# Optimization experiments

Hardware: AMD Instinct MI355X
Metric: run time of the kernel (lower is better)

The kernel has to match this reference:

```python
import jax, jax.numpy as jnp
import numpy as np

B, T, C = 4, 2048, 1024
H = 16
HS = C // H

def setup_inputs() -> dict:
    key = jax.random.key(0)
    ks = jax.random.split(key, 5)
    s = 0.02
    return {
        "x": jax.random.normal(ks[0], (B, T, C), dtype=jnp.float32),
        "c_attn_w": jax.random.normal(ks[1], (C, 3 * C), dtype=jnp.float32) * s,
        "c_attn_b": jax.random.normal(ks[2], (3 * C,), dtype=jnp.float32) * s,
        "c_proj_w": jax.random.normal(ks[3], (C, C), dtype=jnp.float32) * s,
        "c_proj_b": jax.random.normal(ks[4], (C,), dtype=jnp.float32) * s,
    }

def reference(x, c_attn_w, c_attn_b, c_proj_w, c_proj_b):
    b, t, c = x.shape
    qkv = x @ c_attn_w + c_attn_b                       # (B,T,3C)
    q, k, v = jnp.split(qkv, 3, axis=2)
    # (B,T,C) -> (B,H,T,hs)
    q = q.reshape(b, t, H, HS).transpose(0, 2, 1, 3)
    k = k.reshape(b, t, H, HS).transpose(0, 2, 1, 3)
    v = v.reshape(b, t, H, HS).transpose(0, 2, 1, 3)
    scale = 1.0 / np.sqrt(HS).astype(np.float32)
    attn = jnp.einsum("bhqd,bhkd->bhqk", q, k) * scale  # (B,H,T,T)
    causal = jnp.tril(jnp.ones((t, t), dtype=bool))
    attn = jnp.where(causal[None, None, :, :], attn, -jnp.inf)
    attn = jax.nn.softmax(attn, axis=-1)
    y = jnp.einsum("bhqk,bhkd->bhqd", attn, v)          # (B,H,T,hs)
    y = y.transpose(0, 2, 1, 3).reshape(b, t, c)        # (B,T,C)
    return y @ c_proj_w + c_proj_b
```

## Files before the change

### kernel.cpp

```cpp
#include <hip/hip_runtime.h>

typedef __attribute__((ext_vector_type(8))) _Float16 h8;
typedef __attribute__((ext_vector_type(4))) _Float16 h4;
typedef __attribute__((ext_vector_type(4))) float f4;
typedef __attribute__((ext_vector_type(16))) float f16x;
typedef __attribute__((ext_vector_type(4))) unsigned u4;

#define MFMA16(a,b,c) __builtin_amdgcn_mfma_f32_16x16x32_f16(a,b,c,0,0,0)
#define MFMA32(a,b,c) __builtin_amdgcn_mfma_f32_32x32x16_f16(a,b,c,0,0,0)

__device__ inline void gload16(const void* g, void* l) {
    __builtin_amdgcn_global_load_lds(
        (const __attribute__((address_space(1))) void*)g,
        (__attribute__((address_space(3))) void*)l, 16, 0, 0);
}

__device__ inline float swap_half(float x) { return __shfl_xor(x, 32, 64); }

__global__ __launch_bounds__(256) void k_f32_to_f16(const float* __restrict__ in,
                                                    _Float16* __restrict__ out, int n4) {
    int i = blockIdx.x * 256 + threadIdx.x;
    if (i < n4) {
        float4 v = ((const float4*)in)[i];
        h4 h;
        h[0] = (_Float16)v.x; h[1] = (_Float16)v.y;
        h[2] = (_Float16)v.z; h[3] = (_Float16)v.w;
        ((h4*)out)[i] = h;
    }
}

__global__ __launch_bounds__(256) void k_transpose_f16(const float* __restrict__ W,
                                                       _Float16* __restrict__ Wt,
                                                       int K, int N) {
    __shared__ float tile[64 * 68];
    const int k0 = blockIdx.x * 64, n0 = blockIdx.y * 64;
    const int t = threadIdx.x;
    const int tr = t >> 4;
    const int tc = t & 15;
#pragma unroll
    for (int i = 0; i < 4; ++i) {
        int r = tr + i * 16;
        float4 v = *(const float4*)(W + (size_t)(k0 + r) * N + n0 + tc * 4);
        *(float4*)(&tile[r * 68 + tc * 4]) = v;
    }
    __syncthreads();
#pragma unroll
    for (int i = 0; i < 4; ++i) {
        int nl = tr + i * 16;
        h4 hv;
#pragma unroll
        for (int j = 0; j < 4; ++j)
            hv[j] = (_Float16)tile[(tc * 4 + j) * 68 + nl];
        *(h4*)(Wt + (size_t)(n0 + nl) * K + k0 + tc * 4) = hv;
    }
}

template <int MODE>
__global__ __launch_bounds__(256) void k_gemm(const _Float16* __restrict__ A,
                                              const _Float16* __restrict__ Bt,
                                              const float* __restrict__ bias,
                                              _Float16* __restrict__ oQ,
                                              _Float16* __restrict__ oK,
                                              _Float16* __restrict__ oV,
                                              float* __restrict__ oF,
                                              int M, int N, int K) {
    __shared__ _Float16 As[3][128 * 32];
    __shared__ _Float16 Bs[3][128 * 32];
    const int tid = threadIdx.x;
    const int lane = tid & 63, wv = tid >> 6;
    const int wm = wv >> 1, wn = wv & 1;
    const int l15 = lane & 15, l4 = lane >> 4;
    const int bm = blockIdx.x * 128, bn = blockIdx.y * 128;
    f4 acc[4][4] = {};

    const int srow = lane >> 2, scol = (lane & 3) * 8;
    const _Float16* Ag = A + (size_t)(bm + srow) * K + scol;
    const _Float16* Bg = Bt + (size_t)(bn + srow) * K + scol;

    auto STAGE = [&](int tile, int s) {
        const size_t ko = (size_t)tile * 32;
#pragma unroll
        for (int j = 0; j < 2; ++j) {
            const int rb_ = (wv * 2 + j) * 16;
            gload16(Ag + (size_t)rb_ * K + ko, &As[s][(wv * 2 + j) * 512]);
            gload16(Bg + (size_t)rb_ * K + ko, &Bs[s][(wv * 2 + j) * 512]);
        }
    };

    const int NT = K >> 5;
    STAGE(0, 0);
    STAGE(1, 1);
    asm volatile("s_waitcnt vmcnt(4)" ::: "memory");
    __builtin_amdgcn_s_barrier();

    int cs = 0;
    for (int t = 0; t < NT; ++t) {
        const int s2 = cs + 2 >= 3 ? cs - 1 : cs + 2;
        const bool pre2 = (t + 2 < NT);
        if (pre2) STAGE(t + 2, s2);

        const _Float16* Ac = As[cs];
        const _Float16* Bc = Bs[cs];
        h8 af[4], bf[4];
#pragma unroll
        for (int i = 0; i < 4; ++i)
            af[i] = *(const h8*)(&Ac[(wm * 64 + i * 16 + l15) * 32 + l4 * 8]);
#pragma unroll
        for (int i = 0; i < 4; ++i)
            bf[i] = *(const h8*)(&Bc[(wn * 64 + i * 16 + l15) * 32 + l4 * 8]);
        __builtin_amdgcn_s_setprio(1);
#pragma unroll
        for (int mi = 0; mi < 4; ++mi)
#pragma unroll
            for (int ni = 0; ni < 4; ++ni)
                acc[mi][ni] = MFMA16(af[mi], bf[ni], acc[mi][ni]);
        __builtin_amdgcn_s_setprio(0);

        if (t + 1 < NT) {
            if (pre2) asm volatile("s_waitcnt vmcnt(4)" ::: "memory");
            else      asm volatile("s_waitcnt vmcnt(0)" ::: "memory");
            __builtin_amdgcn_s_barrier();
        }
        cs = cs + 1 == 3 ? 0 : cs + 1;
    }

#pragma unroll
    for (int mi = 0; mi < 4; ++mi) {
#pragma unroll
        for (int ni = 0; ni < 4; ++ni) {
            int col = bn + wn * 64 + ni * 16 + l15;
            float bv = bias[col];
            int rb = bm + wm * 64 + mi * 16 + l4 * 4;
            if (MODE == 0) {
                int which = col >> 10, n1 = col & 1023;
                int hh = n1 >> 6, dd = n1 & 63;
                if (which == 2) {
                    int b = rb >> 11, tq = rb & 2047;
                    h4 pv;
#pragma unroll
                    for (int i = 0; i < 4; ++i) pv[i] = (_Float16)(acc[mi][ni][i] + bv);
                    *(h4*)(oV + ((size_t)(b * 16 + hh) * 64 + dd) * 2048 + tq) = pv;
                } else {
                    _Float16* dst = which == 0 ? oQ : oK;
                    const float scl = which == 0 ? 0.18033688011112042f : 1.0f;
#pragma unroll
                    for (int i = 0; i < 4; ++i) {
                        int row = rb + i;
                        int b = row >> 11, tq = row & 2047;
                        dst[(((size_t)b * 16 + hh) * 2048 + tq) * 64 + dd] =
                            (_Float16)((acc[mi][ni][i] + bv) * scl);
                    }
                }
            } else {
#pragma unroll
                for (int i = 0; i < 4; ++i)
                    oF[(size_t)(rb + i) * N + col] = acc[mi][ni][i] + bv;
            }
        }
    }
}

#define SWZI(row, cb) ((((row) << 7) + ((cb) ^ ((((row) & 7) << 4)))) >> 1)

__global__ __launch_bounds__(256) void k_attn(const _Float16* __restrict__ Qh,
                                              const _Float16* __restrict__ Kh,
                                              const _Float16* __restrict__ Vt,
                                              _Float16* __restrict__ Yh) {
    __shared__ _Float16 lds[8192];
    const int bid = blockIdx.x;
    const int bh = bid & 63;
    const int qt = 15 - (bid >> 6);
    const int tid = threadIdx.x, w = tid >> 6;
    const int l31 = tid & 31, hi = (tid >> 5) & 1;
    const int h16 = hi * 16, h4o = hi * 4;
    const size_t base = (size_t)bh * 2048 * 64;

    const int qabs = qt * 128 + w * 32 + l31;
    h8 qf[4];
#pragma unroll
    for (int dk = 0; dk < 4; ++dk)
        qf[dk] = *(const h8*)(Qh + base + (size_t)qabs * 64 + dk * 16 + hi * 8);

    f16x O0 = {}, O1 = {};
    float m = -1e30f, l = 0.f;

    const int sr = tid >> 3;
    const int sc8 = (tid & 7) * 8;
    const int scb = (tid & 7) * 16;
    const int kbb = 2 * qt + 1;
    const int kbw = 2 * qt + (w >> 1);

    {
#pragma unroll
        for (int j = 0; j < 2; ++j) {
            int row = j * 32 + sr;
            h8 kv = *(const h8*)(Kh + base + (size_t)row * 64 + sc8);
            h8 vv = *(const h8*)(Vt + base + (size_t)row * 2048 + sc8);
            *(h8*)(&lds[SWZI(row, scb)]) = kv;
            *(h8*)(&lds[4096 + SWZI(row, scb)]) = vv;
        }
    }
    __syncthreads();

    for (int kb = 0; kb <= kbb; ++kb) {
        const bool pre = (kb < kbb);
        h8 kn[2], vn[2];
        if (pre) {
#pragma unroll
            for (int j = 0; j < 2; ++j) {
                int row = j * 32 + sr;
                kn[j] = *(const h8*)(Kh + base + (size_t)((kb + 1) * 64 + row) * 64 + sc8);
                vn[j] = *(const h8*)(Vt + base + (size_t)row * 2048 + (kb + 1) * 64 + sc8);
            }
        }

        if (kb <= kbw) {
            f16x S0 = {}, S1 = {};
            __builtin_amdgcn_s_setprio(1);
#pragma unroll
            for (int dk = 0; dk < 4; ++dk) {
                h8 kf0 = *(const h8*)(&lds[SWZI(l31, dk * 32 + h16)]);
                h8 kf1 = *(const h8*)(&lds[SWZI(32 + l31, dk * 32 + h16)]);
                S0 = MFMA32(kf0, qf[dk], S0);
                S1 = MFMA32(kf1, qf[dk], S1);
            }
            __builtin_amdgcn_s_setprio(0);

            if (kb == kbw) {
#pragma unroll
                for (int r = 0; r < 16; ++r) {
                    int key = kb * 64 + (r & 3) + 8 * (r >> 2) + h4o;
                    if (key > qabs) S0[r] = -1e30f;
                    if (key + 32 > qabs) S1[r] = -1e30f;
                }
            }

            float tr[16];
#pragma unroll
            for (int r = 0; r < 16; ++r) tr[r] = fmaxf(S0[r], S1[r]);
#pragma unroll
            for (int st = 8; st >= 1; st >>= 1)
#pragma unroll
                for (int r = 0; r < st; ++r) tr[r] = fmaxf(tr[r], tr[r + st]);
            float pm = fmaxf(tr[0], swap_half(tr[0]));
            if (!__all(pm - m <= 8.f)) {
                float mnew = fmaxf(m, pm);
                float scl = __builtin_amdgcn_exp2f(m - mnew);
                m = mnew;
                l *= scl;
#pragma unroll
                for (int r = 0; r < 16; ++r) { O0[r] *= scl; O1[r] *= scl; }
            }
#pragma unroll
            for (int r = 0; r < 16; ++r) {
                S0[r] = __builtin_amdgcn_exp2f(S0[r] - m);
                S1[r] = __builtin_amdgcn_exp2f(S1[r] - m);
            }
#pragma unroll
            for (int r = 0; r < 16; ++r) tr[r] = S0[r] + S1[r];
#pragma unroll
            for (int st = 8; st >= 1; st >>= 1)
#pragma unroll
                for (int r = 0; r < st; ++r) tr[r] += tr[r + st];
            l += tr[0] + swap_half(tr[0]);

            h8 pb[4];
#pragma unroll
            for (int kk = 0; kk < 4; ++kk) {
                const int bb = (kk & 1) * 8;
                unsigned W0, W1, W2, W3;
                if (kk < 2) {
                    W0 = __builtin_bit_cast(unsigned, __builtin_amdgcn_cvt_pkrtz(S0[bb + 0], S0[bb + 1]));
                    W1 = __builtin_bit_cast(unsigned, __builtin_amdgcn_cvt_pkrtz(S0[bb + 2], S0[bb + 3]));
                    W2 = __builtin_bit_cast(unsigned, __builtin_amdgcn_cvt_pkrtz(S0[bb + 4], S0[bb + 5]));
                    W3 = __builtin_bit_cast(unsigned, __builtin_amdgcn_cvt_pkrtz(S0[bb + 6], S0[bb + 7]));
                } else {
                    W0 = __builtin_bit_cast(unsigned, __builtin_amdgcn_cvt_pkrtz(S1[bb + 0], S1[bb + 1]));
                    W1 = __builtin_bit_cast(unsigned, __builtin_amdgcn_cvt_pkrtz(S1[bb + 2], S1[bb + 3]));
                    W2 = __builtin_bit_cast(unsigned, __builtin_amdgcn_cvt_pkrtz(S1[bb + 4], S1[bb + 5]));
                    W3 = __builtin_bit_cast(unsigned, __builtin_amdgcn_cvt_pkrtz(S1[bb + 6], S1[bb + 7]));
                }
                unsigned E0 = (unsigned)__shfl_xor((int)(hi ? W0 : W2), 32, 64);
                unsigned E1 = (unsigned)__shfl_xor((int)(hi ? W1 : W3), 32, 64);
                u4 wvv;
                wvv[0] = hi ? E0 : W0;
                wvv[1] = hi ? E1 : W1;
                wvv[2] = hi ? W2 : E0;
                wvv[3] = hi ? W3 : E1;
                pb[kk] = __builtin_bit_cast(h8, wvv);
            }

            __builtin_amdgcn_s_setprio(1);
#pragma unroll
            for (int kk = 0; kk < 4; ++kk) {
                h8 vf0 = *(const h8*)(&lds[4096 + SWZI(l31, kk * 32 + h16)]);
                h8 vf1 = *(const h8*)(&lds[4096 + SWZI(32 + l31, kk * 32 + h16)]);
                O0 = MFMA32(vf0, pb[kk], O0);
                O1 = MFMA32(vf1, pb[kk], O1);
            }
            __builtin_amdgcn_s_setprio(0);
        }

        __syncthreads();
        if (pre) {
#pragma unroll
            for (int j = 0; j < 2; ++j) {
                int row = j * 32 + sr;
                *(h8*)(&lds[SWZI(row, scb)]) = kn[j];
                *(h8*)(&lds[4096 + SWZI(row, scb)]) = vn[j];
            }
            __syncthreads();
        }
    }

    __syncthreads();

    {
        float inv = 1.0f / l;
        const int R = w * 32 + l31;
#pragma unroll
        for (int rr = 0; rr < 4; ++rr) {
            h4 a, b;
#pragma unroll
            for (int q = 0; q < 4; ++q) {
                a[q] = (_Float16)(O0[rr * 4 + q] * inv);
                b[q] = (_Float16)(O1[rr * 4 + q] * inv);
            }
            *(h4*)(&lds[SWZI(R, rr * 16 + hi * 8)]) = a;
            *(h4*)(&lds[SWZI(R, 64 + rr * 16 + hi * 8)]) = b;
        }
    }
    __syncthreads();
    {
        const int b = bh >> 4, head = bh & 15;
        const int row = tid >> 1;
#pragma unroll
        for (int i = 0; i < 4; ++i) {
            int seg = (tid & 1) * 4 + i;
            h8 v = *(const h8*)(&lds[SWZI(row, seg * 16)]);
            *(h8*)(Yh + ((size_t)(b * 2048 + qt * 128 + row)) * 1024 + head * 64 + seg * 8) = v;
        }
    }
}

extern "C" void kernel_launch(void* const* d_in, const int* in_sizes, int n_in,
                              void* d_out, int out_size, void* d_ws, size_t ws_size,
                              hipStream_t stream) {
    const float* x  = (const float*)d_in[0];
    const float* Wa = (const float*)d_in[1];
    const float* ba = (const float*)d_in[2];
    const float* Wp = (const float*)d_in[3];
    const float* bp = (const float*)d_in[4];
    float* out = (float*)d_out;

    _Float16* ws = (_Float16*)d_ws;
    const size_t SZ_X = (size_t)8192 * 1024;
    const size_t SZ_WA = (size_t)3072 * 1024;
    const size_t SZ_WP = (size_t)1024 * 1024;
    const size_t SZ_H = (size_t)64 * 2048 * 64;
    _Float16* xh  = ws;
    _Float16* WaT = xh + SZ_X;
    _Float16* WpT = WaT + SZ_WA;
    _Float16* Qh  = WpT + SZ_WP;
    _Float16* Kh  = Qh + SZ_H;
    _Float16* Vth = Kh + SZ_H;
    _Float16* Yh  = Vth + SZ_H;

    k_f32_to_f16<<<8192, 256, 0, stream>>>(x, xh, (int)(SZ_X / 4));
    k_transpose_f16<<<dim3(16, 48), 256, 0, stream>>>(Wa, WaT, 1024, 3072);
    k_transpose_f16<<<dim3(16, 16), 256, 0, stream>>>(Wp, WpT, 1024, 1024);
    k_gemm<0><<<dim3(64, 24), 256, 0, stream>>>(xh, WaT, ba, Qh, Kh, Vth, nullptr,
                                                8192, 3072, 1024);
    k_attn<<<1024, 256, 0, stream>>>(Qh, Kh, Vth, Yh);
    k_gemm<1><<<dim3(64, 8), 256, 0, stream>>>(Yh, WpT, bp, nullptr, nullptr, nullptr,
                                               out, 8192, 1024, 1024);
}
```

Measured before the change: 182.0 us.

## Use 256x256 tile 512-thread GEMM with 32x32 MFMA for QKV projection

Replaces the QKV projection GEMM with a new kernel that uses 256x256 output tiles, 512 threads, K-tile 64, double-buffered LDS with XOR-swizzled direct global-to-LDS loads, and 32x32x16 MFMA instructions. Workgroup ids are remapped so that consecutive tiles are spread across XCDs. Larger tiles raise arithmetic intensity and cut redundant global loads, at the cost of 128KB of LDS per block and fewer blocks (384) to fill the machine. The output projection keeps the old 128x128 kernel.

```diff
diff --git a/kernel.cpp b/kernel.cpp
--- a/kernel.cpp
+++ b/kernel.cpp
@@ -55,15 +55,117 @@
     }
 }
 
-template <int MODE>
-__global__ __launch_bounds__(256) void k_gemm(const _Float16* __restrict__ A,
-                                              const _Float16* __restrict__ Bt,
-                                              const float* __restrict__ bias,
-                                              _Float16* __restrict__ oQ,
-                                              _Float16* __restrict__ oK,
-                                              _Float16* __restrict__ oV,
-                                              float* __restrict__ oF,
-                                              int M, int N, int K) {
+__global__ __launch_bounds__(512, 2) void k_gemm256(const _Float16* __restrict__ A,
+                                                    const _Float16* __restrict__ Bt,
+                                                    const float* __restrict__ bias,
+                                                    _Float16* __restrict__ oQ,
+                                                    _Float16* __restrict__ oK,
+                                                    _Float16* __restrict__ oV,
+                                                    int K, int nbn) {
+    __shared__ _Float16 As[2][256 * 64];
+    __shared__ _Float16 Bs[2][256 * 64];
+    const int nwg = gridDim.x;
+    const int q8 = nwg >> 3;
+    const int wg = (blockIdx.x & 7) * q8 + (blockIdx.x >> 3);
+    const int bm = (wg / nbn) * 256, bn = (wg % nbn) * 256;
+    const int tid = threadIdx.x, lane = tid & 63, wv = tid >> 6;
+    const int wm = wv >> 2, wn = wv & 3;
+    const int l31 = lane & 31, hi = lane >> 5;
+    const int srow = lane >> 3;
+    const int scol = ((lane & 7) ^ srow) * 8;
+    const _Float16* Ag = A + (size_t)(bm + wv * 8 + srow) * K + scol;
+    const _Float16* Bg = Bt + (size_t)(bn + wv * 8 + srow) * K + scol;
+    f16x acc[4][2] = {};
+
+#pragma unroll
+    for (int j = 0; j < 4; ++j) gload16(Ag + (size_t)j * 64 * K, &As[0][(j * 64 + wv * 8) * 64]);
+#pragma unroll
+    for (int j = 0; j < 4; ++j) gload16(Bg + (size_t)j * 64 * K, &Bs[0][(j * 64 + wv * 8) * 64]);
+    asm volatile("s_waitcnt vmcnt(0)" ::: "memory");
+    __builtin_amdgcn_s_barrier();
+
+    const int NT = K >> 6;
+    int s = 0;
+    for (int t = 0; t < NT; ++t) {
+        const bool pre = (t + 1 < NT);
+        const size_t ko = (size_t)(t + 1) << 6;
+#pragma unroll
+        for (int p = 0; p < 4; ++p) {
+            const int segA = ((p * 2 + hi) ^ (l31 & 7)) * 8;
+            h8 af[4], bf[2];
+#pragma unroll
+            for (int mf = 0; mf < 4; ++mf)
+                af[mf] = *(const h8*)(&As[s][(wm * 128 + mf * 32 + l31) * 64 + segA]);
+#pragma unroll
+            for (int nf = 0; nf < 2; ++nf)
+                bf[nf] = *(const h8*)(&Bs[s][(wn * 64 + nf * 32 + l31) * 64 + segA]);
+            if (pre) {
+                if (p == 0) {
+#pragma unroll
+                    for (int j = 0; j < 4; ++j)
+                        gload16(Ag + (size_t)j * 64 * K + ko, &As[s ^ 1][(j * 64 + wv * 8) * 64]);
+                } else if (p == 1) {
+#pragma unroll
+                    for (int j = 0; j < 4; ++j)
+                        gload16(Bg + (size_t)j * 64 * K + ko, &Bs[s ^ 1][(j * 64 + wv * 8) * 64]);
+                } else if (p == 3) {
+                    asm volatile("s_waitcnt vmcnt(0)" ::: "memory");
+                }
+            }
+            __builtin_amdgcn_s_barrier();
+            __builtin_amdgcn_s_setprio(1);
+#pragma unroll
+            for (int mf = 0; mf < 4; ++mf)
+#pragma unroll
+                for (int nf = 0; nf < 2; ++nf)
+                    acc[mf][nf] = MFMA32(af[mf], bf[nf], acc[mf][nf]);
+            __builtin_amdgcn_s_setprio(0);
+            __builtin_amdgcn_s_barrier();
+        }
+        s ^= 1;
+    }
+
+#pragma unroll
+    for (int mf = 0; mf < 4; ++mf) {
+#pragma unroll
+        for (int nf = 0; nf < 2; ++nf) {
+            const int col = bn + wn * 64 + nf * 32 + l31;
+            const float bv = bias[col];
+            const int which = col >> 10;
+            const int hh = (col & 1023) >> 6, dd = col & 63;
+            const int rbase = bm + wm * 128 + mf * 32 + hi * 4;
+            if (which == 2) {
+#pragma unroll
+                for (int g = 0; g < 4; ++g) {
+                    const int rb = rbase + g * 8;
+                    const int b = rb >> 11, tq = rb & 2047;
+                    h4 pv;
+#pragma unroll
+                    for (int i = 0; i < 4; ++i) pv[i] = (_Float16)(acc[mf][nf][g * 4 + i] + bv);
+                    *(h4*)(oV + ((size_t)(b * 16 + hh) * 64 + dd) * 2048 + tq) = pv;
+                }
+            } else {
+                _Float16* dst = which == 0 ? oQ : oK;
+                const float scl = which == 0 ? 0.18033688011112042f : 1.0f;
+#pragma unroll
+                for (int g = 0; g < 4; ++g)
+#pragma unroll
+                    for (int i = 0; i < 4; ++i) {
+                        const int rb = rbase + g * 8 + i;
+                        const int b = rb >> 11, tq = rb & 2047;
+                        dst[(((size_t)b * 16 + hh) * 2048 + tq) * 64 + dd] =
+                            (_Float16)((acc[mf][nf][g * 4 + i] + bv) * scl);
+                    }
+            }
+        }
+    }
+}
+
+__global__ __launch_bounds__(256) void k_gemm_proj(const _Float16* __restrict__ A,
+                                                   const _Float16* __restrict__ Bt,
+                                                   const float* __restrict__ bias,
+                                                   float* __restrict__ oF,
+                                                   int M, int N, int K) {
     __shared__ _Float16 As[3][128 * 32];
     __shared__ _Float16 Bs[3][128 * 32];
     const int tid = threadIdx.x;
@@ -131,31 +233,9 @@
             int col = bn + wn * 64 + ni * 16 + l15;
             float bv = bias[col];
             int rb = bm + wm * 64 + mi * 16 + l4 * 4;
-            if (MODE == 0) {
-                int which = col >> 10, n1 = col & 1023;
-                int hh = n1 >> 6, dd = n1 & 63;
-                if (which == 2) {
-                    int b = rb >> 11, tq = rb & 2047;
-                    h4 pv;
-#pragma unroll
-                    for (int i = 0; i < 4; ++i) pv[i] = (_Float16)(acc[mi][ni][i] + bv);
-                    *(h4*)(oV + ((size_t)(b * 16 + hh) * 64 + dd) * 2048 + tq) = pv;
-                } else {
-                    _Float16* dst = which == 0 ? oQ : oK;
-                    const float scl = which == 0 ? 0.18033688011112042f : 1.0f;
-#pragma unroll
-                    for (int i = 0; i < 4; ++i) {
-                        int row = rb + i;
-                        int b = row >> 11, tq = row & 2047;
-                        dst[(((size_t)b * 16 + hh) * 2048 + tq) * 64 + dd] =
-                            (_Float16)((acc[mi][ni][i] + bv) * scl);
-                    }
-                }
-            } else {
-#pragma unroll
-                for (int i = 0; i < 4; ++i)
-                    oF[(size_t)(rb + i) * N + col] = acc[mi][ni][i] + bv;
-            }
+#pragma unroll
+            for (int i = 0; i < 4; ++i)
+                oF[(size_t)(rb + i) * N + col] = acc[mi][ni][i] + bv;
         }
     }
 }
@@ -369,9 +449,7 @@
     k_f32_to_f16<<<8192, 256, 0, stream>>>(x, xh, (int)(SZ_X / 4));
     k_transpose_f16<<<dim3(16, 48), 256, 0, stream>>>(Wa, WaT, 1024, 3072);
     k_transpose_f16<<<dim3(16, 16), 256, 0, stream>>>(Wp, WpT, 1024, 1024);
-    k_gemm<0><<<dim3(64, 24), 256, 0, stream>>>(xh, WaT, ba, Qh, Kh, Vth, nullptr,
-                                                8192, 3072, 1024);
+    k_gemm256<<<384, 512, 0, stream>>>(xh, WaT, ba, Qh, Kh, Vth, 1024, 12);
     k_attn<<<1024, 256, 0, stream>>>(Qh, Kh, Vth, Yh);
-    k_gemm<1><<<dim3(64, 8), 256, 0, stream>>>(Yh, WpT, bp, nullptr, nullptr, nullptr,
-                                               out, 8192, 1024, 1024);
-}
+    k_gemm_proj<<<dim3(64, 8), 256, 0, stream>>>(Yh, WpT, bp, out, 8192, 1024, 1024);
+}
```

Result: slower. 188.8 us (+3.7%).
